# Kernel tuning notes

Hardware: AMD Instinct MI355X
Metric: run time of the kernel (lower is better)

The kernel has to match this reference:

```python
import jax, jax.numpy as jnp
import numpy as np
from jax import lax

EPS = 1e-5
NUM_BITS = 8          # activation quantization bits
NUM_BITS_WEIGHT = 8   # weight quantization bits


def fake_quant(x, bits):
    """Uniform min-max quantize-dequantize (per-tensor), STE on round."""
    mn = jnp.min(x)
    mx = jnp.max(x)
    scale = jnp.maximum((mx - mn) / (2 ** bits - 1), jnp.asarray(1e-8, x.dtype))
    q = jnp.round((x - mn) / scale) * scale + mn
    # straight-through estimator: identity gradient through rounding
    return x + lax.stop_gradient(q - x)


def batchnorm(x, gamma, beta, mean, var):
    # x: [N, C, H, W]; stats per channel C (eval mode, running stats)
    inv = gamma / jnp.sqrt(var + EPS)
    return x * inv[None, :, None, None] + (beta - mean * inv)[None, :, None, None]


def qconv(x, w, padding):
    xq = fake_quant(x, NUM_BITS)
    wq = fake_quant(w, NUM_BITS_WEIGHT)
    return lax.conv_general_dilated(
        xq, wq, window_strides=(1, 1), padding=padding,
        dimension_numbers=("NCHW", "OIHW", "NCHW"))


def setup_inputs() -> dict:
    key = jax.random.key(0)
    ks = jax.random.split(key, 8)
    C_in, bn_size, growth = 512, 4, 32
    C_mid = bn_size * growth  # 128
    N, H, W = 64, 28, 28
    x = jax.random.normal(ks[0], (N, C_in, H, W), dtype=jnp.float32)
    gamma1 = jax.random.uniform(ks[1], (C_in,), minval=0.5, maxval=1.5)
    beta1 = jax.random.normal(ks[2], (C_in,)) * 0.1
    mean1 = jax.random.normal(ks[3], (C_in,)) * 0.1
    var1 = jax.random.uniform(ks[4], (C_in,), minval=0.5, maxval=1.5)
    w1 = jax.random.normal(ks[5], (C_mid, C_in, 1, 1)) * (1.0 / np.sqrt(C_in))
    gamma2 = jax.random.uniform(ks[6], (C_mid,), minval=0.5, maxval=1.5)
    beta2 = jax.random.normal(ks[7], (C_mid,)) * 0.1
    mean2 = jax.random.normal(jax.random.fold_in(key, 10), (C_mid,)) * 0.1
    var2 = jax.random.uniform(jax.random.fold_in(key, 11), (C_mid,), minval=0.5, maxval=1.5)
    w2 = jax.random.normal(jax.random.fold_in(key, 12), (growth, C_mid, 3, 3)) * (1.0 / np.sqrt(C_mid * 9))
    return {"x": x, "gamma1": gamma1, "beta1": beta1, "mean1": mean1, "var1": var1,
            "w1": w1, "gamma2": gamma2, "beta2": beta2, "mean2": mean2, "var2": var2,
            "w2": w2}


def reference(x, gamma1, beta1, mean1, var1, w1, gamma2, beta2, mean2, var2, w2):
    h = jax.nn.relu(batchnorm(x, gamma1, beta1, mean1, var1))
    h = qconv(h, w1, padding=((0, 0), (0, 0)))            # 1x1 conv, 512 -> 128
    h = jax.nn.relu(batchnorm(h, gamma2, beta2, mean2, var2))
    h = qconv(h, w2, padding=((1, 1), (1, 1)))            # 3x3 conv, 128 -> 32
    # drop_rate == 0 -> dropout is identity
    return h
```

## Files before the change

### kernel.cpp

```cpp
#include <hip/hip_runtime.h>

typedef unsigned short u16;
typedef unsigned short u16x4 __attribute__((ext_vector_type(4)));
typedef unsigned short u16x8 __attribute__((ext_vector_type(8)));
typedef short bf16x8 __attribute__((ext_vector_type(8)));
typedef float f32x4 __attribute__((ext_vector_type(4)));

#define EPSF 1e-5f

#define NB   64
#define C1   512
#define C2   128
#define C3   32
#define HH   28
#define WW   28
#define HW   784
#define NHW  50176
#define XELEMS 25690112
#define K1_BLOCKS 2048
#define CONV1_BLOCKS 784
#define CONV2_BLOCKS 784

#define WS_BN1I   64
#define WS_BN1B   2112
#define WS_BN2I   4160
#define WS_BN2B   4672
#define WS_WQ1    5376
#define WS_WQ2    136448
#define WS_P1     210176
#define WS_P2     226560
#define WS_PW1    232832
#define WS_PW2    233344
#define WS_H2     233472

__device__ __forceinline__ float bf2f(u16 u) { return __uint_as_float(((unsigned)u) << 16); }
__device__ __forceinline__ u16 f2bf(float f) {
  unsigned x = __float_as_uint(f);
  return (u16)((x + 0x7fffu + ((x >> 16) & 1u)) >> 16);
}
__device__ __forceinline__ float finz(float f) {
  unsigned u = __float_as_uint(f);
  return ((u & 0x7f800000u) == 0x7f800000u) ? 0.0f : f;
}

__device__ __forceinline__ void block_minmax(float& mn, float& mx) {
  for (int m = 32; m; m >>= 1) {
    mn = fminf(mn, __shfl_xor(mn, m));
    mx = fmaxf(mx, __shfl_xor(mx, m));
  }
  __shared__ float wmn[4], wmx[4];
  const int wv = threadIdx.x >> 6;
  if ((threadIdx.x & 63) == 0) { wmn[wv] = mn; wmx[wv] = mx; }
  __syncthreads();
  if (threadIdx.x == 0) {
    mn = fminf(fminf(wmn[0], wmn[1]), fminf(wmn[2], wmn[3]));
    mx = fmaxf(fmaxf(wmx[0], wmx[1]), fmaxf(wmx[2], wmx[3]));
  }
}

__global__ __launch_bounds__(256) void kwA_kernel(const float* g1, const float* be1,
                                                  const float* m1, const float* v1,
                                                  const float* w1,
                                                  const float* g2, const float* be2,
                                                  const float* m2, const float* v2,
                                                  const float* w2, unsigned char* ws) {
  const int t = threadIdx.x;
  const int b = blockIdx.x;
  float2* pw1 = (float2*)(ws + WS_PW1);
  float2* pw2 = (float2*)(ws + WS_PW2);

  if (b == 80) {
    float* bn1i = (float*)(ws + WS_BN1I);
    float* bn1b = (float*)(ws + WS_BN1B);
    float* bn2i = (float*)(ws + WS_BN2I);
    float* bn2b = (float*)(ws + WS_BN2B);
    for (int c = t; c < C1; c += 256) {
      float inv = g1[c] / sqrtf(v1[c] + EPSF);
      bn1i[c] = inv;
      bn1b[c] = be1[c] - m1[c] * inv;
    }
    if (t < C2) {
      float inv = g2[t] / sqrtf(v2[t] + EPSF);
      bn2i[t] = inv;
      bn2b[t] = be2[t] - m2[t] * inv;
    }
    return;
  }

  float mn = 3.4e38f, mx = -3.4e38f;
  if (b < 64) {
    f32x4 v = *(const f32x4*)(w1 + b * 1024 + t * 4);
#pragma unroll
    for (int j = 0; j < 4; j++) {
      float f = finz(v[j]); mn = fminf(mn, f); mx = fmaxf(mx, f);
    }
    block_minmax(mn, mx);
    if (t == 0) pw1[b] = make_float2(mn, mx);
  } else {
    const int base = (b - 64) * 2304;
#pragma unroll
    for (int j = 0; j < 9; j++) {
      float f = finz(w2[base + t + j * 256]); mn = fminf(mn, f); mx = fmaxf(mx, f);
    }
    block_minmax(mn, mx);
    if (t == 0) pw2[b - 64] = make_float2(mn, mx);
  }
}

__global__ __launch_bounds__(256) void kwB_kernel(const float* w1, const float* w2,
                                                  unsigned char* ws) {
  const float2* pw1 = (const float2*)(ws + WS_PW1);
  const float2* pw2 = (const float2*)(ws + WS_PW2);
  u16* wq1 = (u16*)(ws + WS_WQ1);
  u16* wq2 = (u16*)(ws + WS_WQ2);
  const int t = threadIdx.x;
  const int b = blockIdx.x;
  __shared__ float bc[2];

  if (b < 64) {
    if (t < 64) {
      float2 p = pw1[t];
      float mn = p.x, mx = p.y;
      for (int m = 32; m; m >>= 1) {
        mn = fminf(mn, __shfl_xor(mn, m));
        mx = fmaxf(mx, __shfl_xor(mx, m));
      }
      if (t == 0) { bc[0] = mn; bc[1] = mx; }
    }
    __syncthreads();
    const float mn = bc[0];
    const float s = fmaxf((bc[1] - mn) / 255.0f, 1e-8f);
    const float rs = 1.0f / s;
    f32x4 v = *(const f32x4*)(w1 + b * 1024 + t * 4);
    u16x4 o;
#pragma unroll
    for (int j = 0; j < 4; j++)
      o[j] = f2bf(fmaf(rintf((finz(v[j]) - mn) * rs), s, mn));
    *(u16x4*)(wq1 + b * 1024 + t * 4) = o;
  } else {
    if (t < 64) {
      float2 p = (t < 16) ? pw2[t] : make_float2(3.4e38f, -3.4e38f);
      float mn = p.x, mx = p.y;
      for (int m = 32; m; m >>= 1) {
        mn = fminf(mn, __shfl_xor(mn, m));
        mx = fmaxf(mx, __shfl_xor(mx, m));
      }
      if (t == 0) { bc[0] = mn; bc[1] = mx; }
    }
    __syncthreads();
    const float mn = bc[0];
    const float s = fmaxf((bc[1] - mn) / 255.0f, 1e-8f);
    const float rs = 1.0f / s;
    const int base = (b - 64) * 2304;
#pragma unroll
    for (int j = 0; j < 9; j++) {
      int o = base + t + j * 256;
      int tap = o >> 12;
      int rem = o & 4095;
      float f = finz(w2[rem * 9 + tap]);
      wq2[o] = f2bf(fmaf(rintf((f - mn) * rs), s, mn));
    }
  }
}

__global__ __launch_bounds__(256) void k1_minmax(const float* __restrict__ x, unsigned char* ws) {
  const float* bn1i = (const float*)(ws + WS_BN1I);
  const float* bn1b = (const float*)(ws + WS_BN1B);
  float2* p1 = (float2*)(ws + WS_P1);
  int gid = blockIdx.x * blockDim.x + threadIdx.x;
  int stride = gridDim.x * blockDim.x;
  const int ngroups = XELEMS / 4;
  float mn = 3.4e38f, mx = 0.0f;
  for (int i = gid; i < ngroups; i += stride) {
    int base = i * 4;
    int c = (base / HW) & (C1 - 1);
    float inv = bn1i[c], bb = bn1b[c];
    f32x4 u = *((const f32x4*)x + i);
#pragma unroll
    for (int j = 0; j < 4; j++) {
      float f = fmaxf(fmaf(u[j], inv, bb), 0.0f);
      mn = fminf(mn, f); mx = fmaxf(mx, f);
    }
  }
  block_minmax(mn, mx);
  if (threadIdx.x == 0) p1[blockIdx.x] = make_float2(mn, mx);
}

__global__ __launch_bounds__(256) void conv1_kernel(const float* __restrict__ x,
                                                    unsigned char* ws) {
  const float* bn1i = (const float*)(ws + WS_BN1I);
  const float* bn1b = (const float*)(ws + WS_BN1B);
  const float* bn2i = (const float*)(ws + WS_BN2I);
  const float* bn2b = (const float*)(ws + WS_BN2B);
  const u16* wq1 = (const u16*)(ws + WS_WQ1);
  const float2* p1 = (const float2*)(ws + WS_P1);
  float2* p2 = (float2*)(ws + WS_P2);
  u16* h2 = (u16*)(ws + WS_H2);

  __shared__ __align__(16) u16 Alds[128 * 40];
  __shared__ __align__(16) u16 Blds[64 * 40];
  __shared__ float bc[2];
  __shared__ float wred[8];

  const int t = threadIdx.x;
  const int sp0 = blockIdx.x * 64;

  {
    const f32x4* p4 = (const f32x4*)p1;
    float mn = 3.4e38f, mx = 0.0f;
#pragma unroll
    for (int i = 0; i < 4; i++) {
      f32x4 v = p4[t + i * 256];
      mn = fminf(mn, fminf(v[0], v[2]));
      mx = fmaxf(mx, fmaxf(v[1], v[3]));
    }
    block_minmax(mn, mx);
    if (t == 0) { bc[0] = mn; bc[1] = mx; }
    __syncthreads();
  }
  const float mn1 = bc[0];
  const float s1 = fmaxf((bc[1] - mn1) / 255.0f, 1e-8f);
  const float r1 = 1.0f / s1;

  const int kk = t >> 3;
  const int spA = (t & 7) * 8;
  const int bswz = ((spA >> 3) & 3) * 8;
  const int ga = sp0 + spA;
  const int na = ga / HW, hwa = ga % HW;
  const float* xA = x + na * (C1 * HW) + hwa;

  const int wco = t >> 1;
  const int wko = (t & 1) * 16;
  const int ab0 = wko >> 3;
  const int aswz = (wco >> 3) & 3;

  const int lane = t & 63;
  const int l15 = lane & 15;
  const int q = lane >> 4;
  const int wv = t >> 6;
  const int wy = wv >> 1;
  const int wx = wv & 1;

  f32x4 acc[4][2] = {};

  for (int k0 = 0; k0 < C1; k0 += 32) {
    __syncthreads();
    {
      const u16* src = wq1 + wco * C1 + k0 + wko;
      u16x8 a0 = *(const u16x8*)(src);
      u16x8 a1 = *(const u16x8*)(src + 8);
      *(u16x8*)&Alds[wco * 40 + (((ab0 + 0 + aswz) & 3) << 3)] = a0;
      *(u16x8*)&Alds[wco * 40 + (((ab0 + 1 + aswz) & 3) << 3)] = a1;
    }
    {
      int c = k0 + kk;
      float inv = bn1i[c], bb = bn1b[c];
      f32x4 va0 = *(const f32x4*)(xA + c * HW);
      f32x4 va1 = *(const f32x4*)(xA + c * HW + 4);
      const int col = ((kk + bswz) & 31);
#pragma unroll
      for (int j = 0; j < 4; j++) {
        float f0 = fmaxf(fmaf(va0[j], inv, bb), 0.0f);
        Blds[(spA + j) * 40 + col] = f2bf(fmaf(rintf((f0 - mn1) * r1), s1, mn1));
        float f1 = fmaxf(fmaf(va1[j], inv, bb), 0.0f);
        Blds[(spA + 4 + j) * 40 + col] = f2bf(fmaf(rintf((f1 - mn1) * r1), s1, mn1));
      }
    }
    __syncthreads();
    bf16x8 af[4], bfr[2];
#pragma unroll
    for (int i = 0; i < 4; i++) {
      int R = wy * 64 + i * 16 + l15;
      af[i] = *(const bf16x8*)&Alds[R * 40 + (((q + (R >> 3)) & 3) << 3)];
    }
#pragma unroll
    for (int j = 0; j < 2; j++) {
      int R = wx * 32 + j * 16 + l15;
      bfr[j] = *(const bf16x8*)&Blds[R * 40 + (((q + (R >> 3)) & 3) << 3)];
    }
#pragma unroll
    for (int i = 0; i < 4; i++)
#pragma unroll
      for (int j = 0; j < 2; j++)
        acc[i][j] = __builtin_amdgcn_mfma_f32_16x16x32_bf16(af[i], bfr[j], acc[i][j], 0, 0, 0);
  }

  float lmn = 3.4e38f, lmx = 0.0f;
#pragma unroll
  for (int i = 0; i < 4; i++) {
    int cob = wy * 64 + i * 16 + q * 4;
    f32x4 i2 = *(const f32x4*)&bn2i[cob];
    f32x4 b2 = *(const f32x4*)&bn2b[cob];
#pragma unroll
    for (int j = 0; j < 2; j++) {
      int sp = sp0 + wx * 32 + j * 16 + l15;
      u16x4 v;
#pragma unroll
      for (int r = 0; r < 4; r++) {
        float h = fmaxf(fmaf(acc[i][j][r], i2[r], b2[r]), 0.0f);
        v[r] = f2bf(h);
        lmn = fminf(lmn, h); lmx = fmaxf(lmx, h);
      }
      *(u16x4*)&h2[sp * C2 + cob] = v;
    }
  }
  for (int m = 32; m; m >>= 1) {
    lmn = fminf(lmn, __shfl_xor(lmn, m));
    lmx = fmaxf(lmx, __shfl_xor(lmx, m));
  }
  if (lane == 0) { wred[wv] = lmn; wred[4 + wv] = lmx; }
  __syncthreads();
  if (t == 0) {
    float2 pr;
    pr.x = fminf(fminf(wred[0], wred[1]), fminf(wred[2], wred[3]));
    pr.y = fmaxf(fmaxf(wred[4], wred[5]), fmaxf(wred[6], wred[7]));
    p2[blockIdx.x] = pr;
  }
}

__global__ __launch_bounds__(256) void conv2_kernel(const unsigned char* ws,
                                                    float* __restrict__ out) {
  const u16* wq2 = (const u16*)(ws + WS_WQ2);
  const u16* h2 = (const u16*)(ws + WS_H2);
  const float2* p2 = (const float2*)(ws + WS_P2);
  __shared__ float bc2[2];

  const int t = threadIdx.x;
  {
    float mn = 3.4e38f, mx = 0.0f;
    for (int i = t; i < CONV1_BLOCKS; i += 256) {
      float2 p = p2[i];
      mn = fminf(mn, p.x); mx = fmaxf(mx, p.y);
    }
    block_minmax(mn, mx);
    if (t == 0) { bc2[0] = mn; bc2[1] = mx; }
    __syncthreads();
  }
  const float mn2 = bc2[0];
  const float s2 = fmaxf((bc2[1] - mn2) / 255.0f, 1e-8f);
  const float r2 = 1.0f / s2;

  const int lane = t & 63;
  const int l15 = lane & 15;
  const int q = lane >> 4;
  const int wv = t >> 6;

  const int spf = blockIdx.x * 64 + wv * 16 + l15;
  const int nn = spf / HW;
  const int hwf = spf % HW;
  const int hf = hwf / WW;
  const int wf = hwf % WW;

  f32x4 acc[2] = {};
  bf16x8 bz;
#pragma unroll
  for (int j = 0; j < 8; j++) bz[j] = 0;

  for (int tap = 0; tap < 9; tap++) {
    const int dh = tap / 3 - 1, dw = tap % 3 - 1;
    const u16* wA = wq2 + tap * (C3 * C2);
    unsigned h2i = (unsigned)(hf + dh);
    unsigned w2i = (unsigned)(wf + dw);
    const bool val = (h2i < 28u) && (w2i < 28u);
    const u16* bptr = h2 + ((size_t)(nn * HW + (int)h2i * WW + (int)w2i)) * C2;
#pragma unroll
    for (int ks = 0; ks < C2; ks += 32) {
      bf16x8 a[2], b;
#pragma unroll
      for (int f = 0; f < 2; f++)
        a[f] = *(const bf16x8*)(wA + (f * 16 + l15) * C2 + ks + q * 8);
      if (val) {
        u16x8 hv = *(const u16x8*)(bptr + ks + q * 8);
#pragma unroll
        for (int j = 0; j < 8; j++) {
          float h = bf2f(hv[j]);
          b[j] = (short)f2bf(fmaf(rintf((h - mn2) * r2), s2, mn2));
        }
      } else {
        b = bz;
      }
#pragma unroll
      for (int i = 0; i < 2; i++)
        acc[i] = __builtin_amdgcn_mfma_f32_16x16x32_bf16(a[i], b, acc[i], 0, 0, 0);
    }
  }

#pragma unroll
  for (int i = 0; i < 2; i++) {
    int co = i * 16 + q * 4;
#pragma unroll
    for (int r = 0; r < 4; r++)
      out[(nn * C3 + co + r) * HW + hwf] = acc[i][r];
  }
}

extern "C" void kernel_launch(void* const* d_in, const int* in_sizes, int n_in,
                              void* d_out, int out_size, void* d_ws, size_t ws_size,
                              hipStream_t stream) {
  const float* x  = (const float*)d_in[0];
  const float* g1 = (const float*)d_in[1];
  const float* b1 = (const float*)d_in[2];
  const float* m1 = (const float*)d_in[3];
  const float* v1 = (const float*)d_in[4];
  const float* w1 = (const float*)d_in[5];
  const float* g2 = (const float*)d_in[6];
  const float* b2 = (const float*)d_in[7];
  const float* m2 = (const float*)d_in[8];
  const float* v2 = (const float*)d_in[9];
  const float* w2 = (const float*)d_in[10];
  unsigned char* ws = (unsigned char*)d_ws;
  float* out = (float*)d_out;

  kwA_kernel<<<81, 256, 0, stream>>>(g1, b1, m1, v1, w1, g2, b2, m2, v2, w2, ws);
  kwB_kernel<<<80, 256, 0, stream>>>(w1, w2, ws);
  k1_minmax<<<K1_BLOCKS, 256, 0, stream>>>(x, ws);
  conv1_kernel<<<CONV1_BLOCKS, 256, 0, stream>>>(x, ws);
  conv2_kernel<<<CONV2_BLOCKS, 256, 0, stream>>>(ws, out);
}
```

Baseline: 254.1 us.

## Widen conv1 spatial tile and hoist h2 quantization into separate pass

Conv1 now processes 128 spatial positions per block instead of 64, doubling MFMA work per weight tile load and halving the block count. The per-tap requantization of h2 inside conv2 is moved into a standalone elementwise kernel that quantizes h2 in place once. This removes redundant quantization arithmetic across the nine 3x3 taps. The cost is an extra kernel launch, an extra read/write pass over h2, and fewer conv1 blocks than compute units, which may leave the GPU underfilled.

```diff
diff --git a/kernel.cpp b/kernel.cpp
--- a/kernel.cpp
+++ b/kernel.cpp
@@ -18,8 +18,9 @@
 #define NHW  50176
 #define XELEMS 25690112
 #define K1_BLOCKS 2048
-#define CONV1_BLOCKS 784
+#define CONV1_BLOCKS 392
 #define CONV2_BLOCKS 784
+#define K2Q_BLOCKS 3136
 
 #define WS_BN1I   64
 #define WS_BN1B   2112
@@ -198,12 +199,12 @@
   u16* h2 = (u16*)(ws + WS_H2);
 
   __shared__ __align__(16) u16 Alds[128 * 40];
-  __shared__ __align__(16) u16 Blds[64 * 40];
+  __shared__ __align__(16) u16 Blds[128 * 40];
   __shared__ float bc[2];
   __shared__ float wred[8];
 
   const int t = threadIdx.x;
-  const int sp0 = blockIdx.x * 64;
+  const int sp0 = blockIdx.x * 128;
 
   {
     const f32x4* p4 = (const f32x4*)p1;
@@ -224,10 +225,13 @@
 
   const int kk = t >> 3;
   const int spA = (t & 7) * 8;
-  const int bswz = ((spA >> 3) & 3) * 8;
-  const int ga = sp0 + spA;
+  const int spB = 64 + spA;
+  const int ga = sp0 + spA, gb = sp0 + spB;
   const int na = ga / HW, hwa = ga % HW;
+  const int nb = gb / HW, hwb = gb % HW;
   const float* xA = x + na * (C1 * HW) + hwa;
+  const float* xB = x + nb * (C1 * HW) + hwb;
+  const int colg = (kk & 7) + 8 * ((((kk >> 3) + (spA >> 3))) & 3);
 
   const int wco = t >> 1;
   const int wko = (t & 1) * 16;
@@ -241,7 +245,7 @@
   const int wy = wv >> 1;
   const int wx = wv & 1;
 
-  f32x4 acc[4][2] = {};
+  f32x4 acc[4][4] = {};
 
   for (int k0 = 0; k0 < C1; k0 += 32) {
     __syncthreads();
@@ -257,31 +261,36 @@
       float inv = bn1i[c], bb = bn1b[c];
       f32x4 va0 = *(const f32x4*)(xA + c * HW);
       f32x4 va1 = *(const f32x4*)(xA + c * HW + 4);
-      const int col = ((kk + bswz) & 31);
+      f32x4 vb0 = *(const f32x4*)(xB + c * HW);
+      f32x4 vb1 = *(const f32x4*)(xB + c * HW + 4);
 #pragma unroll
       for (int j = 0; j < 4; j++) {
         float f0 = fmaxf(fmaf(va0[j], inv, bb), 0.0f);
-        Blds[(spA + j) * 40 + col] = f2bf(fmaf(rintf((f0 - mn1) * r1), s1, mn1));
+        Blds[(spA + j) * 40 + colg] = f2bf(fmaf(rintf((f0 - mn1) * r1), s1, mn1));
         float f1 = fmaxf(fmaf(va1[j], inv, bb), 0.0f);
-        Blds[(spA + 4 + j) * 40 + col] = f2bf(fmaf(rintf((f1 - mn1) * r1), s1, mn1));
+        Blds[(spA + 4 + j) * 40 + colg] = f2bf(fmaf(rintf((f1 - mn1) * r1), s1, mn1));
+        float g0 = fmaxf(fmaf(vb0[j], inv, bb), 0.0f);
+        Blds[(spB + j) * 40 + colg] = f2bf(fmaf(rintf((g0 - mn1) * r1), s1, mn1));
+        float g1v = fmaxf(fmaf(vb1[j], inv, bb), 0.0f);
+        Blds[(spB + 4 + j) * 40 + colg] = f2bf(fmaf(rintf((g1v - mn1) * r1), s1, mn1));
       }
     }
     __syncthreads();
-    bf16x8 af[4], bfr[2];
+    bf16x8 af[4], bfr[4];
 #pragma unroll
     for (int i = 0; i < 4; i++) {
       int R = wy * 64 + i * 16 + l15;
       af[i] = *(const bf16x8*)&Alds[R * 40 + (((q + (R >> 3)) & 3) << 3)];
     }
 #pragma unroll
-    for (int j = 0; j < 2; j++) {
-      int R = wx * 32 + j * 16 + l15;
+    for (int j = 0; j < 4; j++) {
+      int R = wx * 64 + j * 16 + l15;
       bfr[j] = *(const bf16x8*)&Blds[R * 40 + (((q + (R >> 3)) & 3) << 3)];
     }
 #pragma unroll
     for (int i = 0; i < 4; i++)
 #pragma unroll
-      for (int j = 0; j < 2; j++)
+      for (int j = 0; j < 4; j++)
         acc[i][j] = __builtin_amdgcn_mfma_f32_16x16x32_bf16(af[i], bfr[j], acc[i][j], 0, 0, 0);
   }
 
@@ -292,8 +301,8 @@
     f32x4 i2 = *(const f32x4*)&bn2i[cob];
     f32x4 b2 = *(const f32x4*)&bn2b[cob];
 #pragma unroll
-    for (int j = 0; j < 2; j++) {
-      int sp = sp0 + wx * 32 + j * 16 + l15;
+    for (int j = 0; j < 4; j++) {
+      int sp = sp0 + wx * 64 + j * 16 + l15;
       u16x4 v;
 #pragma unroll
       for (int r = 0; r < 4; r++) {
@@ -318,13 +327,10 @@
   }
 }
 
-__global__ __launch_bounds__(256) void conv2_kernel(const unsigned char* ws,
-                                                    float* __restrict__ out) {
-  const u16* wq2 = (const u16*)(ws + WS_WQ2);
-  const u16* h2 = (const u16*)(ws + WS_H2);
+__global__ __launch_bounds__(256) void k2q_kernel(unsigned char* ws) {
+  u16* h2 = (u16*)(ws + WS_H2);
   const float2* p2 = (const float2*)(ws + WS_P2);
-  __shared__ float bc2[2];
-
+  __shared__ float bc[2];
   const int t = threadIdx.x;
   {
     float mn = 3.4e38f, mx = 0.0f;
@@ -333,13 +339,30 @@
       mn = fminf(mn, p.x); mx = fmaxf(mx, p.y);
     }
     block_minmax(mn, mx);
-    if (t == 0) { bc2[0] = mn; bc2[1] = mx; }
-    __syncthreads();
-  }
-  const float mn2 = bc2[0];
-  const float s2 = fmaxf((bc2[1] - mn2) / 255.0f, 1e-8f);
+    if (t == 0) { bc[0] = mn; bc[1] = mx; }
+    __syncthreads();
+  }
+  const float mn2 = bc[0];
+  const float s2 = fmaxf((bc[1] - mn2) / 255.0f, 1e-8f);
   const float r2 = 1.0f / s2;
 
+  const int idx = blockIdx.x * 256 + t;
+  u16x8 v = ((u16x8*)h2)[idx];
+  u16x8 o;
+#pragma unroll
+  for (int j = 0; j < 8; j++) {
+    float h = bf2f(v[j]);
+    o[j] = f2bf(fmaf(rintf((h - mn2) * r2), s2, mn2));
+  }
+  ((u16x8*)h2)[idx] = o;
+}
+
+__global__ __launch_bounds__(256) void conv2_kernel(const unsigned char* ws,
+                                                    float* __restrict__ out) {
+  const u16* wq2 = (const u16*)(ws + WS_WQ2);
+  const u16* h2 = (const u16*)(ws + WS_H2);
+
+  const int t = threadIdx.x;
   const int lane = t & 63;
   const int l15 = lane & 15;
   const int q = lane >> 4;
@@ -369,16 +392,7 @@
 #pragma unroll
       for (int f = 0; f < 2; f++)
         a[f] = *(const bf16x8*)(wA + (f * 16 + l15) * C2 + ks + q * 8);
-      if (val) {
-        u16x8 hv = *(const u16x8*)(bptr + ks + q * 8);
-#pragma unroll
-        for (int j = 0; j < 8; j++) {
-          float h = bf2f(hv[j]);
-          b[j] = (short)f2bf(fmaf(rintf((h - mn2) * r2), s2, mn2));
-        }
-      } else {
-        b = bz;
-      }
+      b = val ? *(const bf16x8*)(bptr + ks + q * 8) : bz;
 #pragma unroll
       for (int i = 0; i < 2; i++)
         acc[i] = __builtin_amdgcn_mfma_f32_16x16x32_bf16(a[i], b, acc[i], 0, 0, 0);
@@ -415,5 +429,6 @@
   kwB_kernel<<<80, 256, 0, stream>>>(w1, w2, ws);
   k1_minmax<<<K1_BLOCKS, 256, 0, stream>>>(x, ws);
   conv1_kernel<<<CONV1_BLOCKS, 256, 0, stream>>>(x, ws);
+  k2q_kernel<<<K2Q_BLOCKS, 256, 0, stream>>>(ws);
   conv2_kernel<<<CONV2_BLOCKS, 256, 0, stream>>>(ws, out);
 }
```

After: 259.6 us. 2.2% more time.

## Double tile width in conv1, double-buffer LDS with register prefetch, remap conv2 blocks

Applied to the files above, without the earlier changes.

Conv1 now gives each block 128 spatial positions instead of 64, so every weight tile loaded into LDS is reused across twice as many columns and half as many blocks are launched. The K loop double-buffers LDS and prefetches the next step's weights and activations into registers, which removes one barrier per iteration and overlaps global loads with MFMA work. The initial min/max reduction now runs as an LDS tree over the shared buffers. Conv2 block indices are permuted, likely to spread neighbouring spatial tiles across XCDs or caches. In exchange, register and LDS use per block rise and only 392 blocks launch, which may lower occupancy.

```diff
diff --git a/kernel.cpp b/kernel.cpp
--- a/kernel.cpp
+++ b/kernel.cpp
@@ -18,7 +18,7 @@
 #define NHW  50176
 #define XELEMS 25690112
 #define K1_BLOCKS 2048
-#define CONV1_BLOCKS 784
+#define CONV1_BLOCKS 392
 #define CONV2_BLOCKS 784
 
 #define WS_BN1I   64
@@ -197,15 +197,17 @@
   float2* p2 = (float2*)(ws + WS_P2);
   u16* h2 = (u16*)(ws + WS_H2);
 
-  __shared__ __align__(16) u16 Alds[128 * 40];
-  __shared__ __align__(16) u16 Blds[64 * 40];
+  __shared__ __align__(16) u16 Alds[2][128 * 40];
+  __shared__ __align__(16) u16 Blds[2][128 * 40];
   __shared__ float bc[2];
   __shared__ float wred[8];
 
   const int t = threadIdx.x;
-  const int sp0 = blockIdx.x * 64;
+  const int sp0 = blockIdx.x * 128;
 
   {
+    float* rmn = (float*)&Alds[0][0];
+    float* rmx = (float*)&Blds[0][0];
     const f32x4* p4 = (const f32x4*)p1;
     float mn = 3.4e38f, mx = 0.0f;
 #pragma unroll
@@ -214,8 +216,13 @@
       mn = fminf(mn, fminf(v[0], v[2]));
       mx = fmaxf(mx, fmaxf(v[1], v[3]));
     }
-    block_minmax(mn, mx);
-    if (t == 0) { bc[0] = mn; bc[1] = mx; }
+    rmn[t] = mn; rmx[t] = mx;
+    __syncthreads();
+    for (int s = 128; s > 0; s >>= 1) {
+      if (t < s) { rmn[t] = fminf(rmn[t], rmn[t + s]); rmx[t] = fmaxf(rmx[t], rmx[t + s]); }
+      __syncthreads();
+    }
+    if (t == 0) { bc[0] = rmn[0]; bc[1] = rmx[0]; }
     __syncthreads();
   }
   const float mn1 = bc[0];
@@ -224,10 +231,13 @@
 
   const int kk = t >> 3;
   const int spA = (t & 7) * 8;
-  const int bswz = ((spA >> 3) & 3) * 8;
-  const int ga = sp0 + spA;
+  const int spB = 64 + spA;
+  const int ga = sp0 + spA, gb = sp0 + spB;
   const int na = ga / HW, hwa = ga % HW;
+  const int nb = gb / HW, hwb = gb % HW;
   const float* xA = x + na * (C1 * HW) + hwa;
+  const float* xB = x + nb * (C1 * HW) + hwb;
+  const int colg = (kk & 7) + 8 * ((((kk >> 3) + (spA >> 3))) & 3);
 
   const int wco = t >> 1;
   const int wko = (t & 1) * 16;
@@ -241,48 +251,60 @@
   const int wy = wv >> 1;
   const int wx = wv & 1;
 
-  f32x4 acc[4][2] = {};
-
-  for (int k0 = 0; k0 < C1; k0 += 32) {
-    __syncthreads();
-    {
-      const u16* src = wq1 + wco * C1 + k0 + wko;
-      u16x8 a0 = *(const u16x8*)(src);
-      u16x8 a1 = *(const u16x8*)(src + 8);
-      *(u16x8*)&Alds[wco * 40 + (((ab0 + 0 + aswz) & 3) << 3)] = a0;
-      *(u16x8*)&Alds[wco * 40 + (((ab0 + 1 + aswz) & 3) << 3)] = a1;
-    }
-    {
-      int c = k0 + kk;
-      float inv = bn1i[c], bb = bn1b[c];
-      f32x4 va0 = *(const f32x4*)(xA + c * HW);
-      f32x4 va1 = *(const f32x4*)(xA + c * HW + 4);
-      const int col = ((kk + bswz) & 31);
-#pragma unroll
-      for (int j = 0; j < 4; j++) {
-        float f0 = fmaxf(fmaf(va0[j], inv, bb), 0.0f);
-        Blds[(spA + j) * 40 + col] = f2bf(fmaf(rintf((f0 - mn1) * r1), s1, mn1));
-        float f1 = fmaxf(fmaf(va1[j], inv, bb), 0.0f);
-        Blds[(spA + 4 + j) * 40 + col] = f2bf(fmaf(rintf((f1 - mn1) * r1), s1, mn1));
-      }
-    }
-    __syncthreads();
-    bf16x8 af[4], bfr[2];
-#pragma unroll
-    for (int i = 0; i < 4; i++) {
-      int R = wy * 64 + i * 16 + l15;
-      af[i] = *(const bf16x8*)&Alds[R * 40 + (((q + (R >> 3)) & 3) << 3)];
-    }
-#pragma unroll
-    for (int j = 0; j < 2; j++) {
-      int R = wx * 32 + j * 16 + l15;
-      bfr[j] = *(const bf16x8*)&Blds[R * 40 + (((q + (R >> 3)) & 3) << 3)];
-    }
-#pragma unroll
-    for (int i = 0; i < 4; i++)
-#pragma unroll
-      for (int j = 0; j < 2; j++)
-        acc[i][j] = __builtin_amdgcn_mfma_f32_16x16x32_bf16(af[i], bfr[j], acc[i][j], 0, 0, 0);
+  f32x4 acc[4][4] = {};
+
+  u16x8 a0 = *(const u16x8*)(wq1 + wco * C1 + wko);
+  u16x8 a1 = *(const u16x8*)(wq1 + wco * C1 + wko + 8);
+  f32x4 va0 = *(const f32x4*)(xA + kk * HW);
+  f32x4 va1 = *(const f32x4*)(xA + kk * HW + 4);
+  f32x4 vb0 = *(const f32x4*)(xB + kk * HW);
+  f32x4 vb1 = *(const f32x4*)(xB + kk * HW + 4);
+  float inv = bn1i[kk], bb = bn1b[kk];
+
+#pragma unroll 1
+  for (int i = 0; i < 16; i++) {
+    const int cur = i & 1;
+    *(u16x8*)&Alds[cur][wco * 40 + (((ab0 + 0 + aswz) & 3) << 3)] = a0;
+    *(u16x8*)&Alds[cur][wco * 40 + (((ab0 + 1 + aswz) & 3) << 3)] = a1;
+#pragma unroll
+    for (int j = 0; j < 4; j++) {
+      float f0 = fmaxf(fmaf(va0[j], inv, bb), 0.0f);
+      Blds[cur][(spA + j) * 40 + colg] = f2bf(fmaf(rintf((f0 - mn1) * r1), s1, mn1));
+      float f1 = fmaxf(fmaf(va1[j], inv, bb), 0.0f);
+      Blds[cur][(spA + 4 + j) * 40 + colg] = f2bf(fmaf(rintf((f1 - mn1) * r1), s1, mn1));
+      float g0 = fmaxf(fmaf(vb0[j], inv, bb), 0.0f);
+      Blds[cur][(spB + j) * 40 + colg] = f2bf(fmaf(rintf((g0 - mn1) * r1), s1, mn1));
+      float g1v = fmaxf(fmaf(vb1[j], inv, bb), 0.0f);
+      Blds[cur][(spB + 4 + j) * 40 + colg] = f2bf(fmaf(rintf((g1v - mn1) * r1), s1, mn1));
+    }
+    if (i < 15) {
+      const int kn = (i + 1) * 32;
+      a0 = *(const u16x8*)(wq1 + wco * C1 + kn + wko);
+      a1 = *(const u16x8*)(wq1 + wco * C1 + kn + wko + 8);
+      const int c = kn + kk;
+      va0 = *(const f32x4*)(xA + c * HW);
+      va1 = *(const f32x4*)(xA + c * HW + 4);
+      vb0 = *(const f32x4*)(xB + c * HW);
+      vb1 = *(const f32x4*)(xB + c * HW + 4);
+      inv = bn1i[c]; bb = bn1b[c];
+    }
+    __syncthreads();
+    bf16x8 af[4], bfr[4];
+#pragma unroll
+    for (int ii = 0; ii < 4; ii++) {
+      int R = wy * 64 + ii * 16 + l15;
+      af[ii] = *(const bf16x8*)&Alds[cur][R * 40 + (((q + (R >> 3)) & 3) << 3)];
+    }
+#pragma unroll
+    for (int j = 0; j < 4; j++) {
+      int R = wx * 64 + j * 16 + l15;
+      bfr[j] = *(const bf16x8*)&Blds[cur][R * 40 + (((q + (R >> 3)) & 3) << 3)];
+    }
+#pragma unroll
+    for (int ii = 0; ii < 4; ii++)
+#pragma unroll
+      for (int j = 0; j < 4; j++)
+        acc[ii][j] = __builtin_amdgcn_mfma_f32_16x16x32_bf16(af[ii], bfr[j], acc[ii][j], 0, 0, 0);
   }
 
   float lmn = 3.4e38f, lmx = 0.0f;
@@ -292,8 +314,8 @@
     f32x4 i2 = *(const f32x4*)&bn2i[cob];
     f32x4 b2 = *(const f32x4*)&bn2b[cob];
 #pragma unroll
-    for (int j = 0; j < 2; j++) {
-      int sp = sp0 + wx * 32 + j * 16 + l15;
+    for (int j = 0; j < 4; j++) {
+      int sp = sp0 + wx * 64 + j * 16 + l15;
       u16x4 v;
 #pragma unroll
       for (int r = 0; r < 4; r++) {
@@ -345,7 +367,9 @@
   const int q = lane >> 4;
   const int wv = t >> 6;
 
-  const int spf = blockIdx.x * 64 + wv * 16 + l15;
+  const int B = blockIdx.x;
+  const int sblk = (B & 7) * 98 + (B >> 3);
+  const int spf = sblk * 64 + wv * 16 + l15;
   const int nn = spf / HW;
   const int hwf = spf % HW;
   const int hf = hwf / WW;
```

Result: faster. 248.3 us (median of 2 runs) (-2.3%).
